# Performance work log

Hardware: AMD Instinct MI355X
Metric: run time of the kernel (lower is better)

Reference implementation:

```python
import jax, jax.numpy as jnp
import numpy as np

I4_CLIP = 7.0
NUM_HEADS = 16
NUM_KV_HEADS = 4
HEAD_DIM = 64
ROPE_BASE = 10000.0


def fake_quant_i4(w):
    # per-row int4 symmetric fake quantization with straight-through estimator
    row_max = jnp.maximum(jnp.max(jnp.abs(w), axis=-1, keepdims=True), 1e-8)
    scale = row_max / I4_CLIP
    w_deq = jnp.clip(jnp.round(w / scale), -I4_CLIP, I4_CLIP) * scale
    return w + jax.lax.stop_gradient(w_deq - w)


def rms_norm(x):
    eps = jnp.asarray(jnp.finfo(x.dtype).eps, x.dtype)
    return x * jax.lax.rsqrt(jnp.mean(x * x, axis=-1, keepdims=True) + eps)


def rope_cos_sin(seqlen, dtype):
    inv_freq = 1.0 / (ROPE_BASE ** (jnp.arange(0, HEAD_DIM, 2, dtype=jnp.float32) / HEAD_DIM))
    freqs = jnp.outer(jnp.arange(seqlen, dtype=jnp.float32), inv_freq)  # [S, hd/2]
    return jnp.cos(freqs).astype(dtype), jnp.sin(freqs).astype(dtype)


def apply_rotary(x, cos, sin):
    # x: [B, H, S, hd]; cos/sin: [S, hd/2] broadcast over B, H
    half = x.shape[-1] // 2
    x1, x2 = x[..., :half], x[..., half:]
    return jnp.concatenate((x1 * cos + x2 * sin, -x1 * sin + x2 * cos), axis=-1)


def setup_inputs() -> dict:
    key = jax.random.key(0)
    ks = jax.random.split(key, 6)
    dim = NUM_HEADS * HEAD_DIM
    kv_dim = NUM_KV_HEADS * HEAD_DIM
    return {
        "x": jax.random.normal(ks[0], (2, 2048, dim), jnp.float32),
        "w_q": jax.random.normal(ks[1], (dim, dim), jnp.float32) * 0.02,
        "w_k": jax.random.normal(ks[2], (kv_dim, dim), jnp.float32) * 0.02,
        "w_v": jax.random.normal(ks[3], (kv_dim, dim), jnp.float32) * 0.02,
        "w_proj": jax.random.normal(ks[4], (dim, dim), jnp.float32) * 0.02,
        "q_gain": jnp.ones((NUM_HEADS,), jnp.float32),
    }


def reference(x, w_q, w_k, w_v, w_proj, q_gain):
    bsz, seqlen, dim = x.shape
    rep = NUM_HEADS // NUM_KV_HEADS

    wq, wk, wv, wp = (fake_quant_i4(w) for w in (w_q, w_k, w_v, w_proj))

    # projections: F.linear(x, W) = x @ W.T -> [B, S, out]; split heads -> [B, H, S, hd]
    q = (x @ wq.T).reshape(bsz, seqlen, NUM_HEADS, HEAD_DIM).transpose(0, 2, 1, 3)
    k = (x @ wk.T).reshape(bsz, seqlen, NUM_KV_HEADS, HEAD_DIM).transpose(0, 2, 1, 3)
    v = (x @ wv.T).reshape(bsz, seqlen, NUM_KV_HEADS, HEAD_DIM).transpose(0, 2, 1, 3)

    q, k = rms_norm(q), rms_norm(k)
    cos, sin = rope_cos_sin(seqlen, q.dtype)
    q = apply_rotary(q, cos, sin)
    k = apply_rotary(k, cos, sin)
    q = q * q_gain.astype(q.dtype)[None, :, None, None]

    # GQA: expand kv heads
    k = jnp.repeat(k, rep, axis=1)
    v = jnp.repeat(v, rep, axis=1)

    # causal SDPA
    scale = 1.0 / np.sqrt(HEAD_DIM)
    scores = jnp.einsum("bhqd,bhkd->bhqk", q, k) * scale
    causal = jnp.tril(jnp.ones((seqlen, seqlen), dtype=bool))
    scores = jnp.where(causal, scores, jnp.asarray(-jnp.inf, scores.dtype))
    attn = jax.nn.softmax(scores, axis=-1)
    y = jnp.einsum("bhqk,bhkd->bhqd", attn, v)

    y = y.transpose(0, 2, 1, 3).reshape(bsz, seqlen, dim)
    return y @ wp.T
```

## Files before the change

kernel.cpp:

```cpp
#include <hip/hip_runtime.h>


typedef __bf16 bf16x8 __attribute__((ext_vector_type(8)));
typedef float  f32x4  __attribute__((ext_vector_type(4)));
typedef float  f32x16 __attribute__((ext_vector_type(16)));
typedef int    i32x4  __attribute__((ext_vector_type(4)));

__device__ __forceinline__ unsigned short f2bf(float f) {
  __bf16 h = (__bf16)f;
  return __builtin_bit_cast(unsigned short, h);
}

__global__ void prep(const float* __restrict__ wq, const float* __restrict__ wk,
                     const float* __restrict__ wv, const float* __restrict__ wp,
                     const float* __restrict__ x,
                     unsigned short* __restrict__ wqkv,
                     unsigned short* __restrict__ wpb,
                     unsigned short* __restrict__ x_bf) {
  int bid = blockIdx.x;
  int t = threadIdx.x;
  if (bid >= 2560) {
    int i = ((bid - 2560) * 256 + t) * 4;
    float4 f = *(const float4*)(x + i);
    ushort4 o;
    o.x = f2bf(f.x); o.y = f2bf(f.y); o.z = f2bf(f.z); o.w = f2bf(f.w);
    *(ushort4*)(x_bf + i) = o;
    return;
  }
  int row = bid;
  const float* s;
  unsigned short* d;
  if (row < 1024)      { s = wq + (size_t)row * 1024;          d = wqkv + (size_t)row * 1024; }
  else if (row < 1280) { s = wk + (size_t)(row - 1024) * 1024; d = wqkv + (size_t)row * 1024; }
  else if (row < 1536) { s = wv + (size_t)(row - 1280) * 1024; d = wqkv + (size_t)row * 1024; }
  else                 { s = wp + (size_t)(row - 1536) * 1024; d = wpb + (size_t)(row - 1536) * 1024; }
  float4 v = *(const float4*)(s + t * 4);
  float mx = fmaxf(fmaxf(fabsf(v.x), fabsf(v.y)), fmaxf(fabsf(v.z), fabsf(v.w)));
#pragma unroll
  for (int m = 1; m < 64; m <<= 1) mx = fmaxf(mx, __shfl_xor(mx, m));
  __shared__ float smx[4];
  if ((t & 63) == 0) smx[t >> 6] = mx;
  __syncthreads();
  mx = fmaxf(fmaxf(smx[0], smx[1]), fmaxf(smx[2], smx[3]));
  mx = fmaxf(mx, 1e-8f);
  float scale = mx / 7.0f;
  float q0 = fminf(fmaxf(rintf(v.x / scale), -7.0f), 7.0f);
  float q1 = fminf(fmaxf(rintf(v.y / scale), -7.0f), 7.0f);
  float q2 = fminf(fmaxf(rintf(v.z / scale), -7.0f), 7.0f);
  float q3 = fminf(fmaxf(rintf(v.w / scale), -7.0f), 7.0f);
  ushort4 o;
  o.x = f2bf(q0 * scale); o.y = f2bf(q1 * scale);
  o.z = f2bf(q2 * scale); o.w = f2bf(q3 * scale);
  *(ushort4*)(d + t * 4) = o;
}

#define GLDS(g, l)                                                            \
  __builtin_amdgcn_global_load_lds((const __attribute__((address_space(1))) void*)(g), \
                                   (__attribute__((address_space(3))) void*)(l), 16, 0, 0)

__global__ __launch_bounds__(512, 4) void gemm_bt(
    const unsigned short* __restrict__ A, const unsigned short* __restrict__ Bw,
    float* __restrict__ C, int N, int K, int nbn) {
  int bm = blockIdx.x / nbn, bn = blockIdx.x % nbn;
  int tid = threadIdx.x, w = tid >> 6, lane = tid & 63;
  int l15 = lane & 15, lh = lane >> 4;
  __shared__ __align__(16) unsigned short ldsA[2][128 * 64];
  __shared__ __align__(16) unsigned short ldsB[2][128 * 64];
  int wr = w >> 1, wc = w & 1;
  f32x4 zero = {0.f, 0.f, 0.f, 0.f};
  f32x4 acc[2][4];
#pragma unroll
  for (int i = 0; i < 2; i++)
#pragma unroll
    for (int j = 0; j < 4; j++) acc[i][j] = zero;

  int srow = lane >> 3, schunk = (lane & 7) ^ (lane >> 3);
  const unsigned short* gA0 = A  + (size_t)(bm * 128 + srow) * K + schunk * 8;
  const unsigned short* gB0 = Bw + (size_t)(bn * 128 + srow) * K + schunk * 8;

  int nk = K >> 6;
#pragma unroll
  for (int it = 0; it < 2; it++) {
    int seg = w * 2 + it;
    GLDS(gA0 + (size_t)(seg * 8) * K, (unsigned short*)ldsA[0] + seg * 512);
    GLDS(gB0 + (size_t)(seg * 8) * K, (unsigned short*)ldsB[0] + seg * 512);
  }
  __syncthreads();
  int cur = 0;
  for (int kt = 0; kt < nk; kt++) {
    if (kt + 1 < nk) {
      int k0 = (kt + 1) * 64;
#pragma unroll
      for (int it = 0; it < 2; it++) {
        int seg = w * 2 + it;
        GLDS(gA0 + (size_t)(seg * 8) * K + k0, (unsigned short*)ldsA[cur ^ 1] + seg * 512);
        GLDS(gB0 + (size_t)(seg * 8) * K + k0, (unsigned short*)ldsB[cur ^ 1] + seg * 512);
      }
    }
    const unsigned short* cA = ldsA[cur];
    const unsigned short* cB = ldsB[cur];
#pragma unroll
    for (int ks = 0; ks < 2; ks++) {
      bf16x8 af[2], bfr[4];
#pragma unroll
      for (int fm = 0; fm < 2; fm++) {
        int row = wr * 32 + fm * 16 + l15;
        int slot = (ks * 4 + lh) ^ (row & 7);
        af[fm] = *(const bf16x8*)(cA + row * 64 + slot * 8);
      }
#pragma unroll
      for (int fn = 0; fn < 4; fn++) {
        int row = wc * 64 + fn * 16 + l15;
        int slot = (ks * 4 + lh) ^ (row & 7);
        bfr[fn] = *(const bf16x8*)(cB + row * 64 + slot * 8);
      }
#pragma unroll
      for (int fm = 0; fm < 2; fm++)
#pragma unroll
        for (int fn = 0; fn < 4; fn++)
          acc[fm][fn] = __builtin_amdgcn_mfma_f32_16x16x32_bf16(af[fm], bfr[fn], acc[fm][fn], 0, 0, 0);
    }
    __syncthreads();
    cur ^= 1;
  }
#pragma unroll
  for (int fm = 0; fm < 2; fm++) {
    int r0 = bm * 128 + wr * 32 + fm * 16 + lh * 4;
#pragma unroll
    for (int fn = 0; fn < 4; fn++) {
      int c = bn * 128 + wc * 64 + fn * 16 + l15;
#pragma unroll
      for (int reg = 0; reg < 4; reg++)
        C[(size_t)(r0 + reg) * N + c] = acc[fm][fn][reg];
    }
  }
}

__global__ __launch_bounds__(512, 4) void gemm_qkv(
    const unsigned short* __restrict__ A, const unsigned short* __restrict__ Bw,
    const float* __restrict__ gainp,
    unsigned short* __restrict__ qb, unsigned short* __restrict__ kbp,
    unsigned short* __restrict__ vbp) {
  const int K = 1024;
  int bm = blockIdx.x / 12, bn = blockIdx.x % 12;
  int tid = threadIdx.x, w = tid >> 6, lane = tid & 63;
  int l15 = lane & 15, lh = lane >> 4;
  __shared__ __align__(16) unsigned short ldsA[2][128 * 64];
  __shared__ __align__(16) unsigned short ldsB[2][128 * 64];
  int wr = w >> 1, wc = w & 1;
  f32x4 zero = {0.f, 0.f, 0.f, 0.f};
  f32x4 acc[2][4];
#pragma unroll
  for (int i = 0; i < 2; i++)
#pragma unroll
    for (int j = 0; j < 4; j++) acc[i][j] = zero;

  int srow = lane >> 3, schunk = (lane & 7) ^ (lane >> 3);
  const unsigned short* gA0 = A  + (size_t)(bm * 128 + srow) * K + schunk * 8;
  const unsigned short* gB0 = Bw + (size_t)(bn * 128 + srow) * K + schunk * 8;

#pragma unroll
  for (int it = 0; it < 2; it++) {
    int seg = w * 2 + it;
    GLDS(gA0 + (size_t)(seg * 8) * K, (unsigned short*)ldsA[0] + seg * 512);
    GLDS(gB0 + (size_t)(seg * 8) * K, (unsigned short*)ldsB[0] + seg * 512);
  }
  __syncthreads();
  int cur = 0;
  for (int kt = 0; kt < 16; kt++) {
    if (kt + 1 < 16) {
      int k0 = (kt + 1) * 64;
#pragma unroll
      for (int it = 0; it < 2; it++) {
        int seg = w * 2 + it;
        GLDS(gA0 + (size_t)(seg * 8) * K + k0, (unsigned short*)ldsA[cur ^ 1] + seg * 512);
        GLDS(gB0 + (size_t)(seg * 8) * K + k0, (unsigned short*)ldsB[cur ^ 1] + seg * 512);
      }
    }
    const unsigned short* cA = ldsA[cur];
    const unsigned short* cB = ldsB[cur];
#pragma unroll
    for (int ks = 0; ks < 2; ks++) {
      bf16x8 af[2], bfr[4];
#pragma unroll
      for (int fm = 0; fm < 2; fm++) {
        int row = wr * 32 + fm * 16 + l15;
        int slot = (ks * 4 + lh) ^ (row & 7);
        af[fm] = *(const bf16x8*)(cA + row * 64 + slot * 8);
      }
#pragma unroll
      for (int fn = 0; fn < 4; fn++) {
        int row = wc * 64 + fn * 16 + l15;
        int slot = (ks * 4 + lh) ^ (row & 7);
        bfr[fn] = *(const bf16x8*)(cB + row * 64 + slot * 8);
      }
#pragma unroll
      for (int fm = 0; fm < 2; fm++)
#pragma unroll
        for (int fn = 0; fn < 4; fn++)
          acc[fm][fn] = __builtin_amdgcn_mfma_f32_16x16x32_bf16(af[fm], bfr[fn], acc[fm][fn], 0, 0, 0);
    }
    __syncthreads();
    cur ^= 1;
  }

  int hid = bn * 2 + wc;
  int rbase = bm * 128 + wr * 32;
  if (hid >= 20) {
    int vh = hid - 20;
#pragma unroll
    for (int fm = 0; fm < 2; fm++)
#pragma unroll
      for (int reg = 0; reg < 4; reg++) {
        int r = rbase + fm * 16 + lh * 4 + reg;
        int b = r >> 11, s = r & 2047;
        unsigned short* dst = vbp + (((size_t)(b * 4 + vh) * 2048 + s) << 6);
#pragma unroll
        for (int fn = 0; fn < 4; fn++)
          dst[fn * 16 + l15] = f2bf(acc[fm][fn][reg]);
      }
  } else {
    bool isq = hid < 16;
    float gn = isq ? gainp[hid] : 1.0f;
    float invf0 = __expf(-0.28782313662425572f * (float)l15);
    float invf1 = __expf(-0.28782313662425572f * (float)(l15 + 16));
#pragma unroll
    for (int fm = 0; fm < 2; fm++)
#pragma unroll
      for (int reg = 0; reg < 4; reg++) {
        float y0 = acc[fm][0][reg], y1 = acc[fm][1][reg];
        float y2 = acc[fm][2][reg], y3 = acc[fm][3][reg];
        float ss = y0 * y0 + y1 * y1 + y2 * y2 + y3 * y3;
        ss += __shfl_xor(ss, 1); ss += __shfl_xor(ss, 2);
        ss += __shfl_xor(ss, 4); ss += __shfl_xor(ss, 8);
        float rn = rsqrtf(ss * 0.015625f + 1.1920929e-7f);
        y0 *= rn; y1 *= rn; y2 *= rn; y3 *= rn;
        int r = rbase + fm * 16 + lh * 4 + reg;
        int b = r >> 11, s = r & 2047;
        float c0, s0n, c1, s1n;
        __sincosf((float)s * invf0, &s0n, &c0);
        __sincosf((float)s * invf1, &s1n, &c1);
        float o0 = (y0 * c0 + y2 * s0n) * gn;
        float o1 = (y1 * c1 + y3 * s1n) * gn;
        float o2 = (y2 * c0 - y0 * s0n) * gn;
        float o3 = (y3 * c1 - y1 * s1n) * gn;
        unsigned short* dst = isq
          ? qb  + (((size_t)(b * 16 + hid) * 2048 + s) << 6)
          : kbp + (((size_t)(b * 4 + (hid - 16)) * 2048 + s) << 6);
        dst[l15]      = f2bf(o0);
        dst[l15 + 16] = f2bf(o1);
        dst[l15 + 32] = f2bf(o2);
        dst[l15 + 48] = f2bf(o3);
      }
  }
}

__global__ void v_transpose(const unsigned short* __restrict__ vbp,
                            unsigned short* __restrict__ vt) {
  int bid = blockIdx.x;
  int st = bid & 31, bk = bid >> 5;
  __shared__ unsigned short tile[64][72];
  int t = threadIdx.x;
  int sl = t >> 2, d0 = (t & 3) * 16;
  const unsigned short* src = vbp + (((size_t)bk * 2048 + st * 64 + sl) << 6) + d0;
  *(ushort4*)&tile[sl][d0]      = *(const ushort4*)(src);
  *(ushort4*)&tile[sl][d0 + 4]  = *(const ushort4*)(src + 4);
  *(ushort4*)&tile[sl][d0 + 8]  = *(const ushort4*)(src + 8);
  *(ushort4*)&tile[sl][d0 + 12] = *(const ushort4*)(src + 12);
  __syncthreads();
  int d = t >> 2, p0 = (t & 3) * 16;
  unsigned short* dst = vt + ((size_t)bk * 64 + d) * 2048 + st * 64 + p0;
#pragma unroll
  for (int jo = 0; jo < 16; jo += 4) {
    ushort4 a;
#pragma unroll
    for (int j = 0; j < 4; j++)
      ((unsigned short*)&a)[j] = tile[p0 + jo + j][d];
    *(ushort4*)(dst + jo) = a;
  }
}

template<bool MASK>
__device__ __forceinline__ void attn_tile(
    int kv0, int q0, int l31, int hi, float M2,
    const unsigned short* ldsK, const unsigned short* ldsV,
    const bf16x8 (&qf)[4], float& lsum, f32x16 (&o)[2]) {
  const float K2 = 0.18033688011112042f;
  f32x16 sc[2];
#pragma unroll
  for (int i = 0; i < 16; i++) { sc[0][i] = 0.f; sc[1][i] = 0.f; }
#pragma unroll
  for (int ks = 0; ks < 4; ks++) {
    int slot0 = (2 * ks + hi) ^ (l31 & 7);
    bf16x8 kf0 = *(const bf16x8*)(ldsK + l31 * 64 + slot0 * 8);
    int row1 = 32 + l31;
    int slot1 = (2 * ks + hi) ^ (row1 & 7);
    bf16x8 kf1 = *(const bf16x8*)(ldsK + row1 * 64 + slot1 * 8);
    sc[0] = __builtin_amdgcn_mfma_f32_32x32x16_bf16(kf0, qf[ks], sc[0], 0, 0, 0);
    sc[1] = __builtin_amdgcn_mfma_f32_32x32x16_bf16(kf1, qf[ks], sc[1], 0, 0, 0);
  }
  unsigned int Wp[2][4][2];
  float ls = 0.f;
  int rowq = q0 + l31;
#pragma unroll
  for (int fn = 0; fn < 2; fn++)
#pragma unroll
    for (int g = 0; g < 4; g++) {
      float p4[4];
#pragma unroll
      for (int m = 0; m < 4; m++) {
        int r = 4 * g + m;
        float s = __builtin_fmaf(sc[fn][r], K2, -M2);
        if (MASK) {
          int col = kv0 + fn * 32 + m + 8 * g + 4 * hi;
          if (col > rowq) s = -1e30f;
        }
        float p = __builtin_amdgcn_exp2f(s);
        ls += p;
        p4[m] = p;
      }
      asm("v_cvt_pk_bf16_f32 %0, %1, %2" : "=v"(Wp[fn][g][0]) : "v"(p4[0]), "v"(p4[1]));
      asm("v_cvt_pk_bf16_f32 %0, %1, %2" : "=v"(Wp[fn][g][1]) : "v"(p4[2]), "v"(p4[3]));
    }
  lsum += ls;
#pragma unroll
  for (int ksg = 0; ksg < 4; ksg++) {
    int fn = ksg >> 1, e = ksg & 1;
    unsigned int u0 = Wp[fn][2 * e][0], u1 = Wp[fn][2 * e + 1][0];
    unsigned int u2 = Wp[fn][2 * e][1], u3 = Wp[fn][2 * e + 1][1];
    asm("v_permlane32_swap_b32 %0, %1" : "+v"(u0), "+v"(u1));
    asm("v_permlane32_swap_b32 %0, %1" : "+v"(u2), "+v"(u3));
    i32x4 pw;
    pw[0] = (int)u0; pw[1] = (int)u2; pw[2] = (int)u1; pw[3] = (int)u3;
    bf16x8 pf = __builtin_bit_cast(bf16x8, pw);
    int slot0 = (2 * ksg + hi) ^ (l31 & 7);
    bf16x8 v0 = *(const bf16x8*)(ldsV + l31 * 64 + slot0 * 8);
    int row1 = 32 + l31;
    int slot1 = (2 * ksg + hi) ^ (row1 & 7);
    bf16x8 v1 = *(const bf16x8*)(ldsV + row1 * 64 + slot1 * 8);
    o[0] = __builtin_amdgcn_mfma_f32_32x32x16_bf16(pf, v0, o[0], 0, 0, 0);
    o[1] = __builtin_amdgcn_mfma_f32_32x32x16_bf16(pf, v1, o[1], 0, 0, 0);
  }
}

__global__ __launch_bounds__(256, 3) void attn_fwd(
    const unsigned short* __restrict__ qbuf, const unsigned short* __restrict__ kb,
    const unsigned short* __restrict__ vtb, const float* __restrict__ gain,
    unsigned short* __restrict__ ob, unsigned short* __restrict__ pO,
    float* __restrict__ pL) {
  int bid = blockIdx.x;
  int cid = bid >> 5;
  int bh = bid & 31;
  int b = bh >> 4, h = bh & 15;
  int qb = 0, cum = 0;
  for (int q = 0; q < 16; q++) {
    int ncq = (2 * q + 5) >> 2;
    if (cid < cum + ncq) { qb = q; break; }
    cum += ncq;
  }
  int nt = 2 * qb + 2;
  int nc = (2 * qb + 5) >> 2;
  int ch = cid - cum;
  int base = nt / nc, rem = nt % nc;
  int t0 = ch * base + (ch < rem ? ch : rem);
  int t1 = t0 + base + (ch < rem ? 1 : 0);
  bool direct = (nc == 1);

  int tid = threadIdx.x;
  int w = tid >> 6, lane = tid & 63;
  int l31 = lane & 31, hi = lane >> 5;
  int q0 = qb * 128 + w * 32;
  int kvh = h >> 2;
  const unsigned short* Q  = qbuf + (size_t)(b * 16 + h) * (2048 * 64);
  const unsigned short* Kg = kb   + (size_t)(b * 4 + kvh) * (2048 * 64);
  const unsigned short* Vg = vtb  + (size_t)(b * 4 + kvh) * (64 * 2048);

  __shared__ __align__(16) unsigned short ldsK[2][64 * 64];
  __shared__ __align__(16) unsigned short ldsV[2][64 * 64];

  float gn = gain[h];
  float M2 = __builtin_fmaf(fabsf(gn), 1.46f, 0.02f);

  bf16x8 qf[4];
#pragma unroll
  for (int ks = 0; ks < 4; ks++)
    qf[ks] = *(const bf16x8*)(Q + (size_t)(q0 + l31) * 64 + ks * 16 + hi * 8);

  f32x16 o[2];
#pragma unroll
  for (int i = 0; i < 16; i++) { o[0][i] = 0.f; o[1][i] = 0.f; }
  float lsum = 0.f;

  int srow = lane >> 3;
  int schunk = (lane & 7) ^ (lane >> 3);
  int full = q0 >> 6;

#pragma unroll
  for (int it = 0; it < 2; it++) {
    int seg = w * 2 + it;
    GLDS(Kg + (size_t)(t0 * 64 + seg * 8 + srow) * 64 + schunk * 8,
         (unsigned short*)ldsK[0] + seg * 512);
    GLDS(Vg + (size_t)(seg * 8 + srow) * 2048 + t0 * 64 + schunk * 8,
         (unsigned short*)ldsV[0] + seg * 512);
  }
  __syncthreads();
  int cur = 0;
  for (int t = t0; t < t1; t++) {
    int kv0 = t * 64;
    if (t + 1 < t1) {
      int kn = kv0 + 64;
#pragma unroll
      for (int it = 0; it < 2; it++) {
        int seg = w * 2 + it;
        GLDS(Kg + (size_t)(kn + seg * 8 + srow) * 64 + schunk * 8,
             (unsigned short*)ldsK[cur ^ 1] + seg * 512);
        GLDS(Vg + (size_t)(seg * 8 + srow) * 2048 + kn + schunk * 8,
             (unsigned short*)ldsV[cur ^ 1] + seg * 512);
      }
    }
    if (t < full)
      attn_tile<false>(kv0, q0, l31, hi, M2, ldsK[cur], ldsV[cur], qf, lsum, o);
    else if (kv0 <= q0 + 31)
      attn_tile<true>(kv0, q0, l31, hi, M2, ldsK[cur], ldsV[cur], qf, lsum, o);
    __syncthreads();
    cur ^= 1;
  }

  float lred = lsum + __shfl_xor(lsum, 32);
  if (direct) {
    float linv = 1.0f / lred;
#pragma unroll
    for (int r = 0; r < 16; r++) {
      int qr = (r & 3) + 8 * (r >> 2) + 4 * hi;
      float iv = __shfl(linv, qr);
      size_t rb = (size_t)(b * 2048 + q0 + qr) * 1024 + h * 64;
      ob[rb + l31]      = f2bf(o[0][r] * iv);
      ob[rb + 32 + l31] = f2bf(o[1][r] * iv);
    }
  } else {
    int slot = bh * 70 + (cid - 2);
    unsigned short* po = pO + ((size_t)slot << 13);
    float* pl = pL + slot * 128;
    if (lane < 32) pl[w * 32 + l31] = lred;
#pragma unroll
    for (int r = 0; r < 16; r++) {
      int qr = (r & 3) + 8 * (r >> 2) + 4 * hi;
      int row = w * 32 + qr;
      po[row * 64 + l31]      = f2bf(o[0][r]);
      po[row * 64 + 32 + l31] = f2bf(o[1][r]);
    }
  }
}

__global__ __launch_bounds__(128) void attn_finalize(
    const unsigned short* __restrict__ pO, const float* __restrict__ pL,
    unsigned short* __restrict__ ob) {
  int bid = blockIdx.x;
  int qb = 2 + bid % 14;
  int bh = bid / 14;
  int b = bh >> 4, h = bh & 15;
  int cum = 0;
  for (int q = 0; q < 16; q++) {
    if (q == qb) break;
    cum += (2 * q + 5) >> 2;
  }
  int nc = (2 * qb + 5) >> 2;
  int s0 = bh * 70 + (cum - 2);

  int row = threadIdx.x;
  float acc[64];
#pragma unroll
  for (int j = 0; j < 64; j++) acc[j] = 0.f;
  float l = 0.f;
  for (int c = 0; c < nc; c++) {
    const unsigned short* po = pO + (((size_t)(s0 + c)) << 13) + row * 64;
    l += pL[(s0 + c) * 128 + row];
#pragma unroll
    for (int j = 0; j < 8; j++) {
      uint4 u = *(const uint4*)(po + j * 8);
      const unsigned short* us = (const unsigned short*)&u;
#pragma unroll
      for (int e = 0; e < 8; e++) {
        unsigned int bits = (unsigned int)us[e] << 16;
        acc[j * 8 + e] += __builtin_bit_cast(float, bits);
      }
    }
  }
  float inv = 1.0f / l;
  unsigned short* dst = ob + (size_t)(b * 2048 + qb * 128 + row) * 1024 + h * 64;
  unsigned short outv[64];
#pragma unroll
  for (int c = 0; c < 64; c++) outv[c] = f2bf(acc[c] * inv);
#pragma unroll
  for (int j = 0; j < 8; j++)
    *(uint4*)(dst + j * 8) = *(const uint4*)(outv + j * 8);
}

extern "C" void kernel_launch(void* const* d_in, const int* in_sizes, int n_in,
                              void* d_out, int out_size, void* d_ws, size_t ws_size,
                              hipStream_t stream) {
  const float* x    = (const float*)d_in[0];
  const float* w_q  = (const float*)d_in[1];
  const float* w_k  = (const float*)d_in[2];
  const float* w_v  = (const float*)d_in[3];
  const float* w_p  = (const float*)d_in[4];
  const float* gain = (const float*)d_in[5];
  float* out = (float*)d_out;

  char* ws = (char*)d_ws;
  unsigned short* x_bf  = (unsigned short*)ws;
  unsigned short* wqkv  = (unsigned short*)(ws + (8u << 20));
  unsigned short* wp    = (unsigned short*)(ws + (11u << 20));
  unsigned short* qbuf  = (unsigned short*)(ws + (13u << 20));
  unsigned short* kbuf  = (unsigned short*)(ws + (21u << 20));
  unsigned short* vbuf  = (unsigned short*)(ws + (23u << 20));
  unsigned short* vtbuf = (unsigned short*)(ws + (25u << 20));
  unsigned short* aout  = (unsigned short*)(ws + (27u << 20));
  unsigned short* pO    = (unsigned short*)(ws + (35u << 20));
  float*          pL    = (float*)(ws + (73u << 20));

  prep<<<6656, 256, 0, stream>>>(w_q, w_k, w_v, w_p, x, wqkv, wp, x_bf);
  gemm_qkv<<<32 * 12, 512, 0, stream>>>(x_bf, wqkv, gain, qbuf, kbuf, vbuf);
  v_transpose<<<256, 256, 0, stream>>>(vbuf, vtbuf);
  attn_fwd<<<2304, 256, 0, stream>>>(qbuf, kbuf, vtbuf, gain, aout, pO, pL);
  attn_finalize<<<448, 128, 0, stream>>>(pO, pL, aout);
  gemm_bt<<<32 * 8, 512, 0, stream>>>(aout, wp, out, 1024, 1024, 8);
}
```

Baseline: 100.0 us.

## Swizzle GEMM block order, interleave softmax/PV with setprio, raise attention occupancy

```diff
diff --git a/kernel.cpp b/kernel.cpp
--- a/kernel.cpp
+++ b/kernel.cpp
@@ -60,8 +60,10 @@
 
 __global__ __launch_bounds__(512, 4) void gemm_bt(
     const unsigned short* __restrict__ A, const unsigned short* __restrict__ Bw,
-    float* __restrict__ C, int N, int K, int nbn) {
-  int bm = blockIdx.x / nbn, bn = blockIdx.x % nbn;
+    float* __restrict__ C, int N, int K, int nbn, int cpx) {
+  int bidx = blockIdx.x;
+  int swz = (bidx & 7) * cpx + (bidx >> 3);
+  int bm = swz / nbn, bn = swz % nbn;
   int tid = threadIdx.x, w = tid >> 6, lane = tid & 63;
   int l15 = lane & 15, lh = lane >> 4;
   __shared__ __align__(16) unsigned short ldsA[2][128 * 64];
@@ -142,7 +144,9 @@
     unsigned short* __restrict__ qb, unsigned short* __restrict__ kbp,
     unsigned short* __restrict__ vbp) {
   const int K = 1024;
-  int bm = blockIdx.x / 12, bn = blockIdx.x % 12;
+  int bidx = blockIdx.x;
+  int swz = (bidx & 7) * 48 + (bidx >> 3);
+  int bm = swz / 12, bn = swz % 12;
   int tid = threadIdx.x, w = tid >> 6, lane = tid & 63;
   int l15 = lane & 15, lh = lane >> 4;
   __shared__ __align__(16) unsigned short ldsA[2][128 * 64];
@@ -289,6 +293,7 @@
   f32x16 sc[2];
 #pragma unroll
   for (int i = 0; i < 16; i++) { sc[0][i] = 0.f; sc[1][i] = 0.f; }
+  __builtin_amdgcn_s_setprio(1);
 #pragma unroll
   for (int ks = 0; ks < 4; ks++) {
     int slot0 = (2 * ks + hi) ^ (l31 & 7);
@@ -299,11 +304,12 @@
     sc[0] = __builtin_amdgcn_mfma_f32_32x32x16_bf16(kf0, qf[ks], sc[0], 0, 0, 0);
     sc[1] = __builtin_amdgcn_mfma_f32_32x32x16_bf16(kf1, qf[ks], sc[1], 0, 0, 0);
   }
-  unsigned int Wp[2][4][2];
+  __builtin_amdgcn_s_setprio(0);
   float ls = 0.f;
   int rowq = q0 + l31;
 #pragma unroll
-  for (int fn = 0; fn < 2; fn++)
+  for (int fn = 0; fn < 2; fn++) {
+    unsigned int Wp[4][2];
 #pragma unroll
     for (int g = 0; g < 4; g++) {
       float p4[4];
@@ -319,31 +325,34 @@
         ls += p;
         p4[m] = p;
       }
-      asm("v_cvt_pk_bf16_f32 %0, %1, %2" : "=v"(Wp[fn][g][0]) : "v"(p4[0]), "v"(p4[1]));
-      asm("v_cvt_pk_bf16_f32 %0, %1, %2" : "=v"(Wp[fn][g][1]) : "v"(p4[2]), "v"(p4[3]));
-    }
+      asm("v_cvt_pk_bf16_f32 %0, %1, %2" : "=v"(Wp[g][0]) : "v"(p4[0]), "v"(p4[1]));
+      asm("v_cvt_pk_bf16_f32 %0, %1, %2" : "=v"(Wp[g][1]) : "v"(p4[2]), "v"(p4[3]));
+    }
+    __builtin_amdgcn_s_setprio(1);
+#pragma unroll
+    for (int e = 0; e < 2; e++) {
+      int ksg = fn * 2 + e;
+      unsigned int u0 = Wp[2 * e][0], u1 = Wp[2 * e + 1][0];
+      unsigned int u2 = Wp[2 * e][1], u3 = Wp[2 * e + 1][1];
+      asm("v_permlane32_swap_b32 %0, %1" : "+v"(u0), "+v"(u1));
+      asm("v_permlane32_swap_b32 %0, %1" : "+v"(u2), "+v"(u3));
+      i32x4 pw;
+      pw[0] = (int)u0; pw[1] = (int)u2; pw[2] = (int)u1; pw[3] = (int)u3;
+      bf16x8 pf = __builtin_bit_cast(bf16x8, pw);
+      int slot0 = (2 * ksg + hi) ^ (l31 & 7);
+      bf16x8 v0 = *(const bf16x8*)(ldsV + l31 * 64 + slot0 * 8);
+      int row1 = 32 + l31;
+      int slot1 = (2 * ksg + hi) ^ (row1 & 7);
+      bf16x8 v1 = *(const bf16x8*)(ldsV + row1 * 64 + slot1 * 8);
+      o[0] = __builtin_amdgcn_mfma_f32_32x32x16_bf16(pf, v0, o[0], 0, 0, 0);
+      o[1] = __builtin_amdgcn_mfma_f32_32x32x16_bf16(pf, v1, o[1], 0, 0, 0);
+    }
+    __builtin_amdgcn_s_setprio(0);
+  }
   lsum += ls;
-#pragma unroll
-  for (int ksg = 0; ksg < 4; ksg++) {
-    int fn = ksg >> 1, e = ksg & 1;
-    unsigned int u0 = Wp[fn][2 * e][0], u1 = Wp[fn][2 * e + 1][0];
-    unsigned int u2 = Wp[fn][2 * e][1], u3 = Wp[fn][2 * e + 1][1];
-    asm("v_permlane32_swap_b32 %0, %1" : "+v"(u0), "+v"(u1));
-    asm("v_permlane32_swap_b32 %0, %1" : "+v"(u2), "+v"(u3));
-    i32x4 pw;
-    pw[0] = (int)u0; pw[1] = (int)u2; pw[2] = (int)u1; pw[3] = (int)u3;
-    bf16x8 pf = __builtin_bit_cast(bf16x8, pw);
-    int slot0 = (2 * ksg + hi) ^ (l31 & 7);
-    bf16x8 v0 = *(const bf16x8*)(ldsV + l31 * 64 + slot0 * 8);
-    int row1 = 32 + l31;
-    int slot1 = (2 * ksg + hi) ^ (row1 & 7);
-    bf16x8 v1 = *(const bf16x8*)(ldsV + row1 * 64 + slot1 * 8);
-    o[0] = __builtin_amdgcn_mfma_f32_32x32x16_bf16(pf, v0, o[0], 0, 0, 0);
-    o[1] = __builtin_amdgcn_mfma_f32_32x32x16_bf16(pf, v1, o[1], 0, 0, 0);
-  }
-}
-
-__global__ __launch_bounds__(256, 3) void attn_fwd(
+}
+
+__global__ __launch_bounds__(256, 4) void attn_fwd(
     const unsigned short* __restrict__ qbuf, const unsigned short* __restrict__ kb,
     const unsigned short* __restrict__ vtb, const float* __restrict__ gain,
     unsigned short* __restrict__ ob, unsigned short* __restrict__ pO,
@@ -524,5 +533,5 @@
   v_transpose<<<256, 256, 0, stream>>>(vbuf, vtbuf);
   attn_fwd<<<2304, 256, 0, stream>>>(qbuf, kbuf, vtbuf, gain, aout, pO, pL);
   attn_finalize<<<448, 128, 0, stream>>>(pO, pL, aout);
-  gemm_bt<<<32 * 8, 512, 0, stream>>>(aout, wp, out, 1024, 1024, 8);
-}
+  gemm_bt<<<32 * 8, 512, 0, stream>>>(aout, wp, out, 1024, 1024, 8, 32);
+}
```

Result: no change. 98.40 us (-1.6%).
